# Optimization experiments

Hardware: AMD Instinct MI355X
Metric: run time of the kernel (lower is better)

Reference implementation:

```python
import jax, jax.numpy as jnp
import numpy as np

HEADS = 2
NEG_SLOPE = 0.2
EPS = 1e-16


def setup_inputs() -> dict:
    N, E, D, F = 10000, 320000, 128, 16
    key = jax.random.key(0)
    ks = jax.random.split(key, 8)
    return {
        "x": jax.random.normal(ks[0], (N, D), dtype=jnp.float32),
        "edge_index": jax.random.randint(ks[1], (2, E), 0, N, dtype=jnp.int64),
        "edge_attr": jax.random.normal(ks[2], (E, F), dtype=jnp.float32),
        # stacked per-layer params (5 layers), glorot-ish scale
        "weights": jax.random.normal(ks[3], (5, D, HEADS * D), dtype=jnp.float32) * 0.08,
        "atts": jax.random.normal(ks[4], (5, HEADS, 2 * D), dtype=jnp.float32) * 0.08,
        "biases": jnp.zeros((5, D), dtype=jnp.float32),
        "edge_ws": jax.random.normal(ks[5], (5, HEADS * D, F), dtype=jnp.float32) * 0.2,
        "edge_bs": jnp.zeros((5, HEADS * D), dtype=jnp.float32),
    }


def _gat_layer(x, src, dst, edge_attr_full, W, att, b, ew, eb):
    # x: [N, D]; src/dst: [E_tot] (self loops already appended)
    N, D = x.shape
    H = HEADS
    edge_emb = edge_attr_full @ ew.T + eb               # [E_tot, H*D]
    xw = x @ W                                          # [N, H*D]
    xj = xw[src].reshape(-1, H, D) + edge_emb.reshape(-1, H, D)  # [E_tot, H, D]
    xi = xw[dst].reshape(-1, H, D)
    att_i, att_j = att[:, :D], att[:, D:]               # [H, D] each
    alpha = jnp.einsum('ehd,hd->eh', xi, att_i) + jnp.einsum('ehd,hd->eh', xj, att_j)
    alpha = jax.nn.leaky_relu(alpha, NEG_SLOPE)
    # segment softmax over destination node (every node has a self loop)
    amax = jax.ops.segment_max(alpha, dst, num_segments=N)   # [N, H]
    ea = jnp.exp(alpha - amax[dst])
    denom = jax.ops.segment_sum(ea, dst, num_segments=N)     # [N, H]
    alpha = ea / (denom[dst] + EPS)
    msg = xj * alpha[..., None]                              # [E_tot, H, D]
    aggr = jax.ops.segment_sum(msg, dst, num_segments=N)     # [N, H, D]
    return aggr.mean(axis=1) + b                             # [N, D]


def reference(x, edge_index, edge_attr, weights, atts, biases, edge_ws, edge_bs):
    N = x.shape[0]
    E = edge_index.shape[1]
    F = edge_attr.shape[1]
    # add self loops (PyG flow: edge_index[0]=source j, edge_index[1]=target i)
    loop = jnp.arange(N, dtype=edge_index.dtype)
    src = jnp.concatenate([edge_index[0], loop])
    dst = jnp.concatenate([edge_index[1], loop])
    edge_attr_full = jnp.concatenate(
        [edge_attr, jnp.zeros((N, F), dtype=edge_attr.dtype)], axis=0)
    h = x
    for l in range(5):
        h = _gat_layer(h, src, dst, edge_attr_full,
                       weights[l], atts[l], biases[l], edge_ws[l], edge_bs[l])
        if l < 4:
            h = jax.nn.relu(h)
    return h
```

## Files before the change

kernel.cpp:

```cpp
#include <hip/hip_runtime.h>
#include <hip/hip_fp16.h>

#define HEADS 2
#define DD 128
#define FF 16
#define HD 256
#define NEG_SLOPE 0.2f
#define EPSV 1e-16f

static __device__ __forceinline__ float rdlanef(float v, int i){
  return __uint_as_float(__builtin_amdgcn_readlane(__float_as_uint(v), i));
}
static __device__ __forceinline__ int rdlanei(int v, int i){
  return __builtin_amdgcn_readlane(v, i);
}

__global__ void k_hist_prec(const int* __restrict__ dst, int* __restrict__ counts,
                            const float* __restrict__ atts, const float* __restrict__ edge_ws,
                            const float* __restrict__ edge_bs, float* __restrict__ c5,
                            int E, int Etot, int ebl){
  if ((int)blockIdx.x >= ebl){
    int l = blockIdx.x - ebl;
    int t = threadIdx.x;
    const float* att = atts    + (size_t)l*HEADS*2*DD;
    const float* ew  = edge_ws + (size_t)l*HD*FF;
    const float* eb  = edge_bs + (size_t)l*HD;
    float* c = c5 + (size_t)l*34;
    if (t < 32){
      int h = t >> 4, f = t & 15;
      float acc = 0.f;
      for (int d = 0; d < DD; d++) acc += att[h*2*DD + DD + d]*ew[(size_t)(h*DD+d)*FF + f];
      c[h*FF + f] = acc;
    } else if (t < 34){
      int h = t - 32;
      float acc = 0.f;
      for (int d = 0; d < DD; d++) acc += att[h*2*DD + DD + d]*eb[h*DD + d];
      c[32 + h] = acc;
    }
    return;
  }
  int e = blockIdx.x*256 + threadIdx.x;
  if (e >= Etot) return;
  int dn = (e < E) ? dst[e] : (e - E);
  atomicAdd(&counts[dn], 1);
}

__global__ __launch_bounds__(1024) void k_scan(const int* __restrict__ counts, int* __restrict__ starts,
                       int* __restrict__ cursor, int N, int Etot){
  __shared__ int s[1024];
  int t = threadIdx.x;
  const int CHN = (N + 1023) / 1024;
  int lo = t*CHN, hi = min(lo+CHN, N);
  int loc = 0;
  for (int i = lo; i < hi; i++) loc += counts[i];
  s[t] = loc;
  __syncthreads();
  for (int off = 1; off < 1024; off <<= 1){
    int v = (t >= off) ? s[t-off] : 0;
    __syncthreads();
    s[t] += v;
    __syncthreads();
  }
  int run = (t == 0) ? 0 : s[t-1];
  for (int i = lo; i < hi; i++){
    starts[i] = run; cursor[i] = run; run += counts[i];
  }
  if (t == 0) starts[N] = Etot;
}

__global__ void k_scatter(const int* __restrict__ dst, int* __restrict__ cursor,
                          int* __restrict__ eids, int E, int Etot){
  int e = blockIdx.x*256 + threadIdx.x;
  if (e >= Etot) return;
  int dn = (e < E) ? dst[e] : (e - E);
  int pos = atomicAdd(&cursor[dn], 1);
  eids[pos] = e;
}

__global__ void k_gather_csr(const int* __restrict__ eids, const int* __restrict__ src,
                             const float* __restrict__ eattr, int* __restrict__ srcC,
                             __half* __restrict__ attrC16, int E, int Etot){
  int i = blockIdx.x*256 + threadIdx.x;
  if (i >= Etot) return;
  int eid = eids[i];
  float a[FF];
  if (eid < E){
    srcC[i] = src[eid];
    const float4* in = (const float4*)&eattr[(size_t)eid*FF];
    float4 q0=in[0], q1=in[1], q2=in[2], q3=in[3];
    a[0]=q0.x; a[1]=q0.y; a[2]=q0.z; a[3]=q0.w;
    a[4]=q1.x; a[5]=q1.y; a[6]=q1.z; a[7]=q1.w;
    a[8]=q2.x; a[9]=q2.y; a[10]=q2.z; a[11]=q2.w;
    a[12]=q3.x; a[13]=q3.y; a[14]=q3.z; a[15]=q3.w;
  } else {
    srcC[i] = eid - E;
    #pragma unroll
    for (int f = 0; f < FF; f++) a[f] = 0.f;
  }
  uint4 pk0, pk1;
  {
    __half2 h0 = __floats2half2_rn(a[0],a[1]),  h1 = __floats2half2_rn(a[2],a[3]);
    __half2 h2 = __floats2half2_rn(a[4],a[5]),  h3 = __floats2half2_rn(a[6],a[7]);
    __half2 h4 = __floats2half2_rn(a[8],a[9]),  h5 = __floats2half2_rn(a[10],a[11]);
    __half2 h6 = __floats2half2_rn(a[12],a[13]),h7 = __floats2half2_rn(a[14],a[15]);
    pk0.x=*(unsigned*)&h0; pk0.y=*(unsigned*)&h1; pk0.z=*(unsigned*)&h2; pk0.w=*(unsigned*)&h3;
    pk1.x=*(unsigned*)&h4; pk1.y=*(unsigned*)&h5; pk1.z=*(unsigned*)&h6; pk1.w=*(unsigned*)&h7;
  }
  uint4* ob = (uint4*)&attrC16[(size_t)i*FF];
  ob[0] = pk0; ob[1] = pk1;
}

__global__ void k_attrdot(const __half* __restrict__ attrC16, const float* __restrict__ c5,
                          float* __restrict__ attrdot, int Etot){
  int i = blockIdx.x*256 + threadIdx.x;
  if (i >= Etot) return;
  const uint4* ap = (const uint4*)&attrC16[(size_t)i*FF];
  uint4 p0 = ap[0], p1 = ap[1];
  float a[FF];
  {
    float2 f;
    f = __half22float2(*(__half2*)&p0.x); a[0]=f.x;  a[1]=f.y;
    f = __half22float2(*(__half2*)&p0.y); a[2]=f.x;  a[3]=f.y;
    f = __half22float2(*(__half2*)&p0.z); a[4]=f.x;  a[5]=f.y;
    f = __half22float2(*(__half2*)&p0.w); a[6]=f.x;  a[7]=f.y;
    f = __half22float2(*(__half2*)&p1.x); a[8]=f.x;  a[9]=f.y;
    f = __half22float2(*(__half2*)&p1.y); a[10]=f.x; a[11]=f.y;
    f = __half22float2(*(__half2*)&p1.z); a[12]=f.x; a[13]=f.y;
    f = __half22float2(*(__half2*)&p1.w); a[14]=f.x; a[15]=f.y;
  }
  #pragma unroll
  for (int l = 0; l < 5; l++){
    const float* cl = c5 + (size_t)l*34;
    float d0 = 0.f, d1 = 0.f;
    #pragma unroll
    for (int f = 0; f < FF; f++){
      d0 = fmaf(a[f], cl[f], d0);
      d1 = fmaf(a[f], cl[FF+f], d1);
    }
    *(float2*)&attrdot[((size_t)l*Etot + i)*2] = make_float2(d0, d1);
  }
}

__global__ __launch_bounds__(256) void k_gemm_xw(const float* __restrict__ h, const float* __restrict__ W,
                         const float* __restrict__ att, __half* __restrict__ xwh,
                         float* __restrict__ sbuf, int N){
  __shared__ float sx[16][DD];
  int r0 = blockIdx.x * 16;
  int rows = min(16, N - r0);
  int t = threadIdx.x;
  for (int idx = t; idx < 16*(DD/4); idx += 256){
    int r = idx >> 5, kq = idx & 31;
    float4 v = make_float4(0.f,0.f,0.f,0.f);
    if (r < rows) v = *(const float4*)&h[(size_t)(r0+r)*DD + kq*4];
    *(float4*)&sx[r][kq*4] = v;
  }
  __syncthreads();
  int tx = t & 63, ty = t >> 6;
  int c0 = tx*4;
  float4 acc[4];
  #pragma unroll
  for (int r = 0; r < 4; r++) acc[r] = make_float4(0.f,0.f,0.f,0.f);
  #pragma unroll 4
  for (int kq = 0; kq < 32; kq++){
    float4 w0 = *(const float4*)&W[(size_t)(kq*4+0)*HD + c0];
    float4 w1 = *(const float4*)&W[(size_t)(kq*4+1)*HD + c0];
    float4 w2 = *(const float4*)&W[(size_t)(kq*4+2)*HD + c0];
    float4 w3 = *(const float4*)&W[(size_t)(kq*4+3)*HD + c0];
    #pragma unroll
    for (int r = 0; r < 4; r++){
      float4 hv = *(const float4*)&sx[ty*4+r][kq*4];
      acc[r].x = fmaf(hv.x, w0.x, acc[r].x); acc[r].y = fmaf(hv.x, w0.y, acc[r].y);
      acc[r].z = fmaf(hv.x, w0.z, acc[r].z); acc[r].w = fmaf(hv.x, w0.w, acc[r].w);
      acc[r].x = fmaf(hv.y, w1.x, acc[r].x); acc[r].y = fmaf(hv.y, w1.y, acc[r].y);
      acc[r].z = fmaf(hv.y, w1.z, acc[r].z); acc[r].w = fmaf(hv.y, w1.w, acc[r].w);
      acc[r].x = fmaf(hv.z, w2.x, acc[r].x); acc[r].y = fmaf(hv.z, w2.y, acc[r].y);
      acc[r].z = fmaf(hv.z, w2.z, acc[r].z); acc[r].w = fmaf(hv.z, w2.w, acc[r].w);
      acc[r].x = fmaf(hv.w, w3.x, acc[r].x); acc[r].y = fmaf(hv.w, w3.y, acc[r].y);
      acc[r].z = fmaf(hv.w, w3.z, acc[r].z); acc[r].w = fmaf(hv.w, w3.w, acc[r].w);
    }
  }
  #pragma unroll
  for (int r = 0; r < 4; r++){
    if (ty*4+r < rows){
      __half2 p0 = __floats2half2_rn(acc[r].x, acc[r].y);
      __half2 p1 = __floats2half2_rn(acc[r].z, acc[r].w);
      uint2 pk;
      pk.x = *(unsigned*)&p0;
      pk.y = *(unsigned*)&p1;
      *(uint2*)&xwh[(size_t)(r0+ty*4+r)*HD + c0] = pk;
    }
  }
  int hsel = tx >> 5;
  int cm = c0 & 127;
  float4 ai = *(const float4*)&att[hsel*2*DD + cm];
  float4 aj = *(const float4*)&att[hsel*2*DD + DD + cm];
  #pragma unroll
  for (int r = 0; r < 4; r++){
    float pi = acc[r].x*ai.x + acc[r].y*ai.y + acc[r].z*ai.z + acc[r].w*ai.w;
    float pj = acc[r].x*aj.x + acc[r].y*aj.y + acc[r].z*aj.z + acc[r].w*aj.w;
    #pragma unroll
    for (int off = 16; off; off >>= 1){
      pi += __shfl_xor(pi, off);
      pj += __shfl_xor(pj, off);
    }
    int row = ty*4 + r;
    if ((tx & 31) == 0 && row < rows){
      sbuf[(size_t)(r0+row)*4 + 0 + hsel] = pi;
      sbuf[(size_t)(r0+row)*4 + 2 + hsel] = pj;
    }
  }
}

#define BB 8
__global__ __launch_bounds__(256) void k_aggr_h(const int* __restrict__ starts, const int* __restrict__ srcC,
                      const __half* __restrict__ attrC16, const float* __restrict__ adL,
                      const float* __restrict__ s, const float* __restrict__ c,
                      const __half* __restrict__ xwh, const float* __restrict__ ew,
                      const float* __restrict__ eb, const float* __restrict__ bias,
                      float* __restrict__ tmph, float* __restrict__ out,
                      int N, int relu, int hh){
  int lane = threadIdx.x & 63, wid = threadIdx.x >> 6;
  int n = blockIdx.x*4 + wid;
  if (n >= N) return;

  float c32h = c[32 + hh];
  float sdh  = s[(size_t)n*4 + hh];
  int st = starts[n];
  int deg = starts[n+1] - st;

  int f2 = lane & 15;
  const __half* xbase = xwh + hh*DD + lane*2;

  float acc0 = 0.f, acc1 = 0.f, ls = 0.f, tacc = 0.f;

  for (int base = 0; base < deg; base += 64){
    int cnt = min(64, deg - base);
    float ee = 0.f; int msrc = 0;
    if (lane < cnt){
      int idx = st + base + lane;
      msrc = srcC[idx];
      float sj = s[(size_t)msrc*4 + 2 + hh];
      float ad = adL[(size_t)idx*2 + hh];
      float x = sdh + sj + c32h + ad;
      x = (x > 0.f) ? x : NEG_SLOPE*x;
      ee = expf(x);
      ls += ee;
    }
    const __half* abase = &attrC16[(size_t)(st+base)*FF + f2];
    int i = 0;
    for (; i + BB <= cnt; i += BB){
      unsigned u[BB];
      float av[BB];
      #pragma unroll
      for (int k = 0; k < BB; k++){
        int sn = rdlanei(msrc, i+k);
        u[k] = *(const unsigned*)(xbase + (size_t)sn*HD);
      }
      #pragma unroll
      for (int k = 0; k < BB; k++) av[k] = __half2float(abase[(size_t)(i+k)*FF]);
      #pragma unroll
      for (int k = 0; k < BB; k++){
        float w = rdlanef(ee, i+k);
        float2 xv = __half22float2(*(__half2*)&u[k]);
        acc0 = fmaf(w, xv.x, acc0);
        acc1 = fmaf(w, xv.y, acc1);
        tacc = fmaf(w, av[k], tacc);
      }
    }
    for (; i < cnt; i++){
      int sn = rdlanei(msrc, i);
      float w = rdlanef(ee, i);
      unsigned u0 = *(const unsigned*)(xbase + (size_t)sn*HD);
      float av0 = __half2float(abase[(size_t)i*FF]);
      float2 xv = __half22float2(*(__half2*)&u0);
      acc0 = fmaf(w, xv.x, acc0);
      acc1 = fmaf(w, xv.y, acc1);
      tacc = fmaf(w, av0, tacc);
    }
  }
  #pragma unroll
  for (int off = 32; off; off >>= 1) ls += __shfl_xor(ls, off);

  int c2 = lane*2;
  float th[FF];
  #pragma unroll
  for (int f = 0; f < FF; f++) th[f] = rdlanef(tacc, f);
  float emb0 = 0.f, emb1 = 0.f;
  {
    const float4* e0p = (const float4*)&ew[(size_t)(hh*DD + c2)*FF];
    const float4* e1p = (const float4*)&ew[(size_t)(hh*DD + c2 + 1)*FF];
    #pragma unroll
    for (int q = 0; q < 4; q++){
      float4 g0 = e0p[q], g1 = e1p[q];
      emb0 = fmaf(th[q*4+0], g0.x, emb0); emb0 = fmaf(th[q*4+1], g0.y, emb0);
      emb0 = fmaf(th[q*4+2], g0.z, emb0); emb0 = fmaf(th[q*4+3], g0.w, emb0);
      emb1 = fmaf(th[q*4+0], g1.x, emb1); emb1 = fmaf(th[q*4+1], g1.y, emb1);
      emb1 = fmaf(th[q*4+2], g1.z, emb1); emb1 = fmaf(th[q*4+3], g1.w, emb1);
    }
  }
  float di = 1.f/(ls + EPSV);
  float2 ebv = *(const float2*)&eb[hh*DD + c2];
  float p0 = di*(acc0 + emb0) + ebv.x;
  float p1 = di*(acc1 + emb1) + ebv.y;
  if (hh == 0){
    *(float2*)&tmph[(size_t)n*DD + c2] = make_float2(p0, p1);
  } else {
    float2 t0 = *(const float2*)&tmph[(size_t)n*DD + c2];
    float2 bv = *(const float2*)&bias[c2];
    float o0 = 0.5f*(t0.x + p0) + bv.x;
    float o1 = 0.5f*(t0.y + p1) + bv.y;
    if (relu){ o0 = fmaxf(o0, 0.f); o1 = fmaxf(o1, 0.f); }
    *(float2*)&out[(size_t)n*DD + c2] = make_float2(o0, o1);
  }
}

extern "C" void kernel_launch(void* const* d_in, const int* in_sizes, int n_in,
                              void* d_out, int out_size, void* d_ws, size_t ws_size,
                              hipStream_t stream){
  const float* x       = (const float*)d_in[0];
  const int*   eidx    = (const int*)d_in[1];
  const float* eattr   = (const float*)d_in[2];
  const float* weights = (const float*)d_in[3];
  const float* atts    = (const float*)d_in[4];
  const float* biases  = (const float*)d_in[5];
  const float* edge_ws = (const float*)d_in[6];
  const float* edge_bs = (const float*)d_in[7];
  const int N = in_sizes[0]/DD;
  const int E = in_sizes[1]/2;
  const int Etot = E + N;
  const int* src = eidx;
  const int* dst = eidx + E;

  char* p = (char*)d_ws;
  auto alloc = [&](size_t bytes){ void* r = (void*)p; p += (bytes + 255) & ~(size_t)255; return r; };
  float*    hA      = (float*)alloc((size_t)N*DD*4);
  float*    hB      = (float*)alloc((size_t)N*DD*4);
  float*    tmph    = (float*)alloc((size_t)N*DD*4);
  __half*   xwh     = (__half*)alloc((size_t)N*HD*2);
  float*    sbuf    = (float*)alloc((size_t)N*4*4);
  int*      starts  = (int*)alloc((size_t)(N+1)*4);
  int*      srcC    = (int*)alloc((size_t)Etot*4);
  int*      eids    = (int*)alloc((size_t)Etot*4);
  __half*   attrC16 = (__half*)alloc((size_t)Etot*FF*2);
  float*    attrdot = (float*)alloc((size_t)5*Etot*2*4);
  float*    c5      = (float*)alloc(5*34*4);

  int* counts = (int*)sbuf;
  int* cursor = (int*)((char*)sbuf + 65536);

  const int ebl = (Etot + 255)/256;

  hipMemsetAsync(counts, 0, (size_t)N*4, stream);
  k_hist_prec<<<ebl+5, 256, 0, stream>>>(dst, counts, atts, edge_ws, edge_bs, c5, E, Etot, ebl);
  k_scan<<<1, 1024, 0, stream>>>(counts, starts, cursor, N, Etot);
  k_scatter<<<ebl, 256, 0, stream>>>(dst, cursor, eids, E, Etot);
  k_gather_csr<<<ebl, 256, 0, stream>>>(eids, src, eattr, srcC, attrC16, E, Etot);
  k_attrdot<<<ebl, 256, 0, stream>>>(attrC16, c5, attrdot, Etot);

  const float* hin = x;
  const int agrid = (N+3)/4;
  for (int l = 0; l < 5; l++){
    const float* W   = weights + (size_t)l*DD*HD;
    const float* att = atts    + (size_t)l*HEADS*2*DD;
    const float* b   = biases  + (size_t)l*DD;
    const float* ew  = edge_ws + (size_t)l*HD*FF;
    const float* eb  = edge_bs + (size_t)l*HD;
    const float* c   = c5 + (size_t)l*34;
    const float* adL = attrdot + (size_t)l*Etot*2;
    float* hout = (l == 4) ? (float*)d_out : ((l & 1) ? hB : hA);
    int relu = (l < 4) ? 1 : 0;

    k_gemm_xw<<<(N+15)/16, 256, 0, stream>>>(hin, W, att, xwh, sbuf, N);
    k_aggr_h<<<agrid, 256, 0, stream>>>(starts, srcC, attrC16, adL, sbuf, c, xwh, ew, eb, b, tmph, hout, N, relu, 0);
    k_aggr_h<<<agrid, 256, 0, stream>>>(starts, srcC, attrC16, adL, sbuf, c, xwh, ew, eb, b, tmph, hout, N, relu, 1);

    hin = hout;
  }
}
```

Baseline: 419.7 us.

## Fuse both heads into one aggregation block and precompute edge attention weights

Replaces the two per-head aggregation launches with one kernel that gives each destination node a 256-thread block. Four waves split the work across heads and even/odd edges, then combine through shared memory, which removes the fp32 tmph round trip. A new per-edge kernel computes leaky-relu and exp attention scores into a half2 buffer before aggregation. Weights are also pre-converted to fp16 so the GEMM loads half the bytes. The cost is an extra launch per layer, fp16 storage of the exp scores and weights (less precision, and exp values can overflow fp16), and one block per node, which may underuse threads on low-degree nodes.

New measurement: 410.1 us. 1.02x faster.

```diff
diff --git a/kernel.cpp b/kernel.cpp
--- a/kernel.cpp
+++ b/kernel.cpp
@@ -14,32 +14,48 @@
 static __device__ __forceinline__ int rdlanei(int v, int i){
   return __builtin_amdgcn_readlane(v, i);
 }
+static __device__ __forceinline__ float4 h4f(uint2 u){
+  float2 f0 = __half22float2(*(__half2*)&u.x);
+  float2 f1 = __half22float2(*(__half2*)&u.y);
+  return make_float4(f0.x, f0.y, f1.x, f1.y);
+}
 
 __global__ void k_hist_prec(const int* __restrict__ dst, int* __restrict__ counts,
                             const float* __restrict__ atts, const float* __restrict__ edge_ws,
-                            const float* __restrict__ edge_bs, float* __restrict__ c5,
+                            const float* __restrict__ edge_bs, const float* __restrict__ weights,
+                            float* __restrict__ c5, __half* __restrict__ wh,
                             int E, int Etot, int ebl){
-  if ((int)blockIdx.x >= ebl){
-    int l = blockIdx.x - ebl;
-    int t = threadIdx.x;
-    const float* att = atts    + (size_t)l*HEADS*2*DD;
-    const float* ew  = edge_ws + (size_t)l*HD*FF;
-    const float* eb  = edge_bs + (size_t)l*HD;
-    float* c = c5 + (size_t)l*34;
-    if (t < 32){
-      int h = t >> 4, f = t & 15;
-      float acc = 0.f;
-      for (int d = 0; d < DD; d++) acc += att[h*2*DD + DD + d]*ew[(size_t)(h*DD+d)*FF + f];
-      c[h*FF + f] = acc;
-    } else if (t < 34){
-      int h = t - 32;
-      float acc = 0.f;
-      for (int d = 0; d < DD; d++) acc += att[h*2*DD + DD + d]*eb[h*DD + d];
-      c[32 + h] = acc;
+  int bid = blockIdx.x;
+  if (bid >= ebl){
+    int k = bid - ebl;
+    if (k < 5){
+      int l = k, t = threadIdx.x;
+      const float* att = atts    + (size_t)l*HEADS*2*DD;
+      const float* ew  = edge_ws + (size_t)l*HD*FF;
+      const float* eb  = edge_bs + (size_t)l*HD;
+      float* c = c5 + (size_t)l*34;
+      if (t < 32){
+        int h = t >> 4, f = t & 15;
+        float acc = 0.f;
+        for (int d = 0; d < DD; d++) acc += att[h*2*DD + DD + d]*ew[(size_t)(h*DD+d)*FF + f];
+        c[h*FF + f] = acc;
+      } else if (t < 34){
+        int h = t - 32;
+        float acc = 0.f;
+        for (int d = 0; d < DD; d++) acc += att[h*2*DD + DD + d]*eb[h*DD + d];
+        c[32 + h] = acc;
+      }
+    } else {
+      int base = (k - 5)*1024 + threadIdx.x*4;
+      float4 w = *(const float4*)&weights[base];
+      __half2 p0 = __floats2half2_rn(w.x, w.y);
+      __half2 p1 = __floats2half2_rn(w.z, w.w);
+      uint2 pk; pk.x = *(unsigned*)&p0; pk.y = *(unsigned*)&p1;
+      *(uint2*)&wh[base] = pk;
     }
     return;
   }
-  int e = blockIdx.x*256 + threadIdx.x;
+  int e = bid*256 + threadIdx.x;
   if (e >= Etot) return;
   int dn = (e < E) ? dst[e] : (e - E);
   atomicAdd(&counts[dn], 1);
@@ -78,7 +94,8 @@
 }
 
 __global__ void k_gather_csr(const int* __restrict__ eids, const int* __restrict__ src,
-                             const float* __restrict__ eattr, int* __restrict__ srcC,
+                             const int* __restrict__ dst, const float* __restrict__ eattr,
+                             int* __restrict__ srcC, int* __restrict__ dstC,
                              __half* __restrict__ attrC16, int E, int Etot){
   int i = blockIdx.x*256 + threadIdx.x;
   if (i >= Etot) return;
@@ -86,6 +103,7 @@
   float a[FF];
   if (eid < E){
     srcC[i] = src[eid];
+    dstC[i] = dst[eid];
     const float4* in = (const float4*)&eattr[(size_t)eid*FF];
     float4 q0=in[0], q1=in[1], q2=in[2], q3=in[3];
     a[0]=q0.x; a[1]=q0.y; a[2]=q0.z; a[3]=q0.w;
@@ -94,6 +112,7 @@
     a[12]=q3.x; a[13]=q3.y; a[14]=q3.z; a[15]=q3.w;
   } else {
     srcC[i] = eid - E;
+    dstC[i] = eid - E;
     #pragma unroll
     for (int f = 0; f < FF; f++) a[f] = 0.f;
   }
@@ -141,7 +160,7 @@
   }
 }
 
-__global__ __launch_bounds__(256) void k_gemm_xw(const float* __restrict__ h, const float* __restrict__ W,
+__global__ __launch_bounds__(256) void k_gemm_xw(const float* __restrict__ h, const __half* __restrict__ Wh,
                          const float* __restrict__ att, __half* __restrict__ xwh,
                          float* __restrict__ sbuf, int N){
   __shared__ float sx[16][DD];
@@ -162,10 +181,10 @@
   for (int r = 0; r < 4; r++) acc[r] = make_float4(0.f,0.f,0.f,0.f);
   #pragma unroll 4
   for (int kq = 0; kq < 32; kq++){
-    float4 w0 = *(const float4*)&W[(size_t)(kq*4+0)*HD + c0];
-    float4 w1 = *(const float4*)&W[(size_t)(kq*4+1)*HD + c0];
-    float4 w2 = *(const float4*)&W[(size_t)(kq*4+2)*HD + c0];
-    float4 w3 = *(const float4*)&W[(size_t)(kq*4+3)*HD + c0];
+    float4 w0 = h4f(*(const uint2*)&Wh[(size_t)(kq*4+0)*HD + c0]);
+    float4 w1 = h4f(*(const uint2*)&Wh[(size_t)(kq*4+1)*HD + c0]);
+    float4 w2 = h4f(*(const uint2*)&Wh[(size_t)(kq*4+2)*HD + c0]);
+    float4 w3 = h4f(*(const uint2*)&Wh[(size_t)(kq*4+3)*HD + c0]);
     #pragma unroll
     for (int r = 0; r < 4; r++){
       float4 hv = *(const float4*)&sx[ty*4+r][kq*4];
@@ -211,42 +230,52 @@
   }
 }
 
+__global__ void k_ea(const int* __restrict__ srcC, const int* __restrict__ dstC,
+                     const float* __restrict__ adL, const float* __restrict__ s,
+                     const float* __restrict__ c, __half2* __restrict__ ea, int Etot){
+  int i = blockIdx.x*256 + threadIdx.x;
+  if (i >= Etot) return;
+  int sn = srcC[i], dn = dstC[i];
+  float2 si = *(const float2*)&s[(size_t)dn*4];
+  float2 sj = *(const float2*)&s[(size_t)sn*4+2];
+  float2 ad = *(const float2*)&adL[(size_t)i*2];
+  float x0 = si.x + sj.x + c[32] + ad.x;
+  float x1 = si.y + sj.y + c[33] + ad.y;
+  x0 = (x0 > 0.f) ? x0 : NEG_SLOPE*x0;
+  x1 = (x1 > 0.f) ? x1 : NEG_SLOPE*x1;
+  ea[i] = __floats2half2_rn(expf(x0), expf(x1));
+}
+
 #define BB 8
-__global__ __launch_bounds__(256) void k_aggr_h(const int* __restrict__ starts, const int* __restrict__ srcC,
-                      const __half* __restrict__ attrC16, const float* __restrict__ adL,
-                      const float* __restrict__ s, const float* __restrict__ c,
+__global__ __launch_bounds__(256) void k_aggr2(const int* __restrict__ starts, const int* __restrict__ srcC,
+                      const __half* __restrict__ attrC16, const __half2* __restrict__ ea,
                       const __half* __restrict__ xwh, const float* __restrict__ ew,
                       const float* __restrict__ eb, const float* __restrict__ bias,
-                      float* __restrict__ tmph, float* __restrict__ out,
-                      int N, int relu, int hh){
-  int lane = threadIdx.x & 63, wid = threadIdx.x >> 6;
-  int n = blockIdx.x*4 + wid;
-  if (n >= N) return;
-
-  float c32h = c[32 + hh];
-  float sdh  = s[(size_t)n*4 + hh];
+                      float* __restrict__ out, int N, int relu){
+  int lane = threadIdx.x & 63, wv = threadIdx.x >> 6;
+  int n = blockIdx.x;
+  int hh = wv >> 1, par = wv & 1;
+
   int st = starts[n];
   int deg = starts[n+1] - st;
+  int cw = (deg + 1 - par) >> 1;
 
   int f2 = lane & 15;
   const __half* xbase = xwh + hh*DD + lane*2;
 
   float acc0 = 0.f, acc1 = 0.f, ls = 0.f, tacc = 0.f;
 
-  for (int base = 0; base < deg; base += 64){
-    int cnt = min(64, deg - base);
+  for (int jb = 0; jb < cw; jb += 64){
+    int cnt = min(64, cw - jb);
     float ee = 0.f; int msrc = 0;
     if (lane < cnt){
-      int idx = st + base + lane;
-      msrc = srcC[idx];
-      float sj = s[(size_t)msrc*4 + 2 + hh];
-      float ad = adL[(size_t)idx*2 + hh];
-      float x = sdh + sj + c32h + ad;
-      x = (x > 0.f) ? x : NEG_SLOPE*x;
-      ee = expf(x);
+      int g = st + 2*(jb + lane) + par;
+      msrc = srcC[g];
+      float2 e2 = __half22float2(ea[g]);
+      ee = hh ? e2.y : e2.x;
       ls += ee;
     }
-    const __half* abase = &attrC16[(size_t)(st+base)*FF + f2];
+    const __half* abase = attrC16 + (size_t)(st + 2*jb + par)*FF + f2;
     int i = 0;
     for (; i + BB <= cnt; i += BB){
       unsigned u[BB];
@@ -257,7 +286,7 @@
         u[k] = *(const unsigned*)(xbase + (size_t)sn*HD);
       }
       #pragma unroll
-      for (int k = 0; k < BB; k++) av[k] = __half2float(abase[(size_t)(i+k)*FF]);
+      for (int k = 0; k < BB; k++) av[k] = __half2float(abase[(size_t)(i+k)*2*FF]);
       #pragma unroll
       for (int k = 0; k < BB; k++){
         float w = rdlanef(ee, i+k);
@@ -271,7 +300,7 @@
       int sn = rdlanei(msrc, i);
       float w = rdlanef(ee, i);
       unsigned u0 = *(const unsigned*)(xbase + (size_t)sn*HD);
-      float av0 = __half2float(abase[(size_t)i*FF]);
+      float av0 = __half2float(abase[(size_t)i*2*FF]);
       float2 xv = __half22float2(*(__half2*)&u0);
       acc0 = fmaf(w, xv.x, acc0);
       acc1 = fmaf(w, xv.y, acc1);
@@ -281,37 +310,61 @@
   #pragma unroll
   for (int off = 32; off; off >>= 1) ls += __shfl_xor(ls, off);
 
+  __shared__ float m_acc[4][64][2];
+  __shared__ float m_t[4][64];
+  __shared__ float m_ls[4];
+  m_acc[wv][lane][0] = acc0;
+  m_acc[wv][lane][1] = acc1;
+  m_t[wv][lane] = tacc;
+  if (lane == 0) m_ls[wv] = ls;
+  __syncthreads();
+  if (wv != 0) return;
+
+  float a00 = m_acc[0][lane][0] + m_acc[1][lane][0];
+  float a01 = m_acc[0][lane][1] + m_acc[1][lane][1];
+  float a10 = m_acc[2][lane][0] + m_acc[3][lane][0];
+  float a11 = m_acc[2][lane][1] + m_acc[3][lane][1];
+  float ls0 = m_ls[0] + m_ls[1];
+  float ls1 = m_ls[2] + m_ls[3];
+  float th0[FF], th1[FF];
+  #pragma unroll
+  for (int f = 0; f < FF; f++){
+    th0[f] = m_t[0][f] + m_t[1][f];
+    th1[f] = m_t[2][f] + m_t[3][f];
+  }
   int c2 = lane*2;
-  float th[FF];
-  #pragma unroll
-  for (int f = 0; f < FF; f++) th[f] = rdlanef(tacc, f);
-  float emb0 = 0.f, emb1 = 0.f;
+  float emb00=0.f, emb01=0.f, emb10=0.f, emb11=0.f;
   {
-    const float4* e0p = (const float4*)&ew[(size_t)(hh*DD + c2)*FF];
-    const float4* e1p = (const float4*)&ew[(size_t)(hh*DD + c2 + 1)*FF];
+    const float4* e00 = (const float4*)&ew[(size_t)(c2)*FF];
+    const float4* e01 = (const float4*)&ew[(size_t)(c2+1)*FF];
+    const float4* e10 = (const float4*)&ew[(size_t)(DD+c2)*FF];
+    const float4* e11 = (const float4*)&ew[(size_t)(DD+c2+1)*FF];
     #pragma unroll
     for (int q = 0; q < 4; q++){
-      float4 g0 = e0p[q], g1 = e1p[q];
-      emb0 = fmaf(th[q*4+0], g0.x, emb0); emb0 = fmaf(th[q*4+1], g0.y, emb0);
-      emb0 = fmaf(th[q*4+2], g0.z, emb0); emb0 = fmaf(th[q*4+3], g0.w, emb0);
-      emb1 = fmaf(th[q*4+0], g1.x, emb1); emb1 = fmaf(th[q*4+1], g1.y, emb1);
-      emb1 = fmaf(th[q*4+2], g1.z, emb1); emb1 = fmaf(th[q*4+3], g1.w, emb1);
-    }
-  }
-  float di = 1.f/(ls + EPSV);
-  float2 ebv = *(const float2*)&eb[hh*DD + c2];
-  float p0 = di*(acc0 + emb0) + ebv.x;
-  float p1 = di*(acc1 + emb1) + ebv.y;
-  if (hh == 0){
-    *(float2*)&tmph[(size_t)n*DD + c2] = make_float2(p0, p1);
-  } else {
-    float2 t0 = *(const float2*)&tmph[(size_t)n*DD + c2];
-    float2 bv = *(const float2*)&bias[c2];
-    float o0 = 0.5f*(t0.x + p0) + bv.x;
-    float o1 = 0.5f*(t0.y + p1) + bv.y;
-    if (relu){ o0 = fmaxf(o0, 0.f); o1 = fmaxf(o1, 0.f); }
-    *(float2*)&out[(size_t)n*DD + c2] = make_float2(o0, o1);
-  }
+      float4 g00 = e00[q], g01 = e01[q], g10 = e10[q], g11 = e11[q];
+      emb00 = fmaf(th0[q*4+0],g00.x,emb00); emb00 = fmaf(th0[q*4+1],g00.y,emb00);
+      emb00 = fmaf(th0[q*4+2],g00.z,emb00); emb00 = fmaf(th0[q*4+3],g00.w,emb00);
+      emb01 = fmaf(th0[q*4+0],g01.x,emb01); emb01 = fmaf(th0[q*4+1],g01.y,emb01);
+      emb01 = fmaf(th0[q*4+2],g01.z,emb01); emb01 = fmaf(th0[q*4+3],g01.w,emb01);
+      emb10 = fmaf(th1[q*4+0],g10.x,emb10); emb10 = fmaf(th1[q*4+1],g10.y,emb10);
+      emb10 = fmaf(th1[q*4+2],g10.z,emb10); emb10 = fmaf(th1[q*4+3],g10.w,emb10);
+      emb11 = fmaf(th1[q*4+0],g11.x,emb11); emb11 = fmaf(th1[q*4+1],g11.y,emb11);
+      emb11 = fmaf(th1[q*4+2],g11.z,emb11); emb11 = fmaf(th1[q*4+3],g11.w,emb11);
+    }
+  }
+  float di0 = 1.f/(ls0 + EPSV);
+  float di1 = 1.f/(ls1 + EPSV);
+  float2 eb0 = *(const float2*)&eb[c2];
+  float2 eb1 = *(const float2*)&eb[DD + c2];
+  float p00 = di0*(a00 + emb00) + eb0.x;
+  float p01 = di0*(a01 + emb01) + eb0.y;
+  float p10 = di1*(a10 + emb10) + eb1.x;
+  float p11 = di1*(a11 + emb11) + eb1.y;
+  float2 bv = *(const float2*)&bias[c2];
+  float o0 = 0.5f*(p00 + p10) + bv.x;
+  float o1 = 0.5f*(p01 + p11) + bv.y;
+  if (relu){ o0 = fmaxf(o0, 0.f); o1 = fmaxf(o1, 0.f); }
+  *(float2*)&out[(size_t)n*DD + c2] = make_float2(o0, o1);
 }
 
 extern "C" void kernel_launch(void* const* d_in, const int* in_sizes, int n_in,
@@ -335,14 +388,16 @@
   auto alloc = [&](size_t bytes){ void* r = (void*)p; p += (bytes + 255) & ~(size_t)255; return r; };
   float*    hA      = (float*)alloc((size_t)N*DD*4);
   float*    hB      = (float*)alloc((size_t)N*DD*4);
-  float*    tmph    = (float*)alloc((size_t)N*DD*4);
   __half*   xwh     = (__half*)alloc((size_t)N*HD*2);
   float*    sbuf    = (float*)alloc((size_t)N*4*4);
   int*      starts  = (int*)alloc((size_t)(N+1)*4);
   int*      srcC    = (int*)alloc((size_t)Etot*4);
+  int*      dstC    = (int*)alloc((size_t)Etot*4);
   int*      eids    = (int*)alloc((size_t)Etot*4);
   __half*   attrC16 = (__half*)alloc((size_t)Etot*FF*2);
   float*    attrdot = (float*)alloc((size_t)5*Etot*2*4);
+  __half2*  eaBuf   = (__half2*)alloc((size_t)Etot*4);
+  __half*   wh      = (__half*)alloc((size_t)5*DD*HD*2);
   float*    c5      = (float*)alloc(5*34*4);
 
   int* counts = (int*)sbuf;
@@ -351,16 +406,16 @@
   const int ebl = (Etot + 255)/256;
 
   hipMemsetAsync(counts, 0, (size_t)N*4, stream);
-  k_hist_prec<<<ebl+5, 256, 0, stream>>>(dst, counts, atts, edge_ws, edge_bs, c5, E, Etot, ebl);
+  k_hist_prec<<<ebl+165, 256, 0, stream>>>(dst, counts, atts, edge_ws, edge_bs, weights,
+                                           c5, wh, E, Etot, ebl);
   k_scan<<<1, 1024, 0, stream>>>(counts, starts, cursor, N, Etot);
   k_scatter<<<ebl, 256, 0, stream>>>(dst, cursor, eids, E, Etot);
-  k_gather_csr<<<ebl, 256, 0, stream>>>(eids, src, eattr, srcC, attrC16, E, Etot);
+  k_gather_csr<<<ebl, 256, 0, stream>>>(eids, src, dst, eattr, srcC, dstC, attrC16, E, Etot);
   k_attrdot<<<ebl, 256, 0, stream>>>(attrC16, c5, attrdot, Etot);
 
   const float* hin = x;
-  const int agrid = (N+3)/4;
   for (int l = 0; l < 5; l++){
-    const float* W   = weights + (size_t)l*DD*HD;
+    const __half* Whl = wh + (size_t)l*DD*HD;
     const float* att = atts    + (size_t)l*HEADS*2*DD;
     const float* b   = biases  + (size_t)l*DD;
     const float* ew  = edge_ws + (size_t)l*HD*FF;
@@ -370,9 +425,9 @@
     float* hout = (l == 4) ? (float*)d_out : ((l & 1) ? hB : hA);
     int relu = (l < 4) ? 1 : 0;
 
-    k_gemm_xw<<<(N+15)/16, 256, 0, stream>>>(hin, W, att, xwh, sbuf, N);
-    k_aggr_h<<<agrid, 256, 0, stream>>>(starts, srcC, attrC16, adL, sbuf, c, xwh, ew, eb, b, tmph, hout, N, relu, 0);
-    k_aggr_h<<<agrid, 256, 0, stream>>>(starts, srcC, attrC16, adL, sbuf, c, xwh, ew, eb, b, tmph, hout, N, relu, 1);
+    k_gemm_xw<<<(N+15)/16, 256, 0, stream>>>(hin, Whl, att, xwh, sbuf, N);
+    k_ea<<<ebl, 256, 0, stream>>>(srcC, dstC, adL, sbuf, c, eaBuf, Etot);
+    k_aggr2<<<N, 256, 0, stream>>>(starts, srcC, attrC16, eaBuf, xwh, ew, eb, b, hout, N, relu);
 
     hin = hout;
   }
```
